# Performance work log

Hardware: AMD Instinct MI355X
Metric: run time of the kernel (lower is better)

The kernel has to match this reference:

```python
import jax, jax.numpy as jnp
import numpy as np

N_NODES = 100000
D_FEAT = 128            # per-embedding width; concat of 4 -> 512
INPUT_DIM = 4 * D_FEAT
HIDDEN_DIM = 64
N_SAMPLES = 250000


def _glorot(key, fan_in, fan_out):
    r = np.sqrt(6.0 / fan_in).astype(np.float32)
    return jax.random.uniform(key, (fan_in, fan_out), minval=-r, maxval=r, dtype=jnp.float32)


def setup_inputs() -> dict:
    key = jax.random.key(0)
    k1, k2, k3, k4, k5 = jax.random.split(key, 5)
    input1 = jax.random.normal(k1, (N_NODES, D_FEAT), dtype=jnp.float32)
    input2 = jax.random.normal(k2, (N_NODES, D_FEAT), dtype=jnp.float32)
    train_sample = jax.random.randint(k3, (N_SAMPLES, 2), 0, N_NODES, dtype=jnp.int64)
    w1 = _glorot(k4, INPUT_DIM, HIDDEN_DIM)
    b1 = jnp.zeros((HIDDEN_DIM,), dtype=jnp.float32)
    w2 = _glorot(k5, HIDDEN_DIM, 1)
    return {"input1": input1, "input2": input2, "train_sample": train_sample,
            "w1": w1, "b1": b1, "w2": w2}


def reference(input1, input2, train_sample, w1, b1, w2):
    src = train_sample[:, 0]
    dst = train_sample[:, 1]
    # four gathers + concat -> [E, 4*D_FEAT]
    h = jnp.concatenate([input1[src], input1[dst], input2[src], input2[dst]], axis=1)
    x = jax.nn.relu(h @ w1 + b1)          # [E, HIDDEN_DIM]
    return x @ w2                          # [E, 1]
```

## Files before the change

### kernel.cpp

```cpp
#include <hip/hip_runtime.h>
#include <hip/hip_bf16.h>

#define NN  100000
#define DF  128
#define HD  64
#define NS  250000


typedef __attribute__((ext_vector_type(8))) short bfrag;
typedef __attribute__((ext_vector_type(4))) float ffrag;

__device__ __forceinline__ unsigned short bf16bits(float f) {
    __hip_bfloat16 b = __float2bfloat16(f);
    return *(unsigned short*)&b;
}
__device__ __forceinline__ unsigned pack2(float a, float b) {
    return (unsigned)bf16bits(a) | ((unsigned)bf16bits(b) << 16);
}
__device__ __forceinline__ float bflo(unsigned u) {
    union { unsigned i; float f; } c; c.i = u << 16; return c.f;
}
__device__ __forceinline__ float bfhi(unsigned u) {
    union { unsigned i; float f; } c; c.i = u & 0xffff0000u; return c.f;
}

__global__ __launch_bounds__(256) void prep_w1_kernel(
    const float* __restrict__ w1, unsigned short* __restrict__ Bf)
{
    const int gid  = blockIdx.x * 256 + threadIdx.x;
    const int lane = gid & 63;
    const int ks   = (gid >> 6) & 7;
    const int tn   = gid >> 9;

    const int n     = tn * 16 + (lane & 15);
    const int kbase = ks * 32 + (lane >> 4) * 8;
    const int col   = n & 63;

    uint4 u;
    unsigned p[4];
    #pragma unroll
    for (int jp = 0; jp < 4; ++jp) {
        float v[2];
        #pragma unroll
        for (int h = 0; h < 2; ++h) {
            const int k = kbase + jp * 2 + h;
            const int row = ((k >= 128) ? 256 : 0) + ((n >= 64) ? 128 : 0) + (k & 127);
            v[h] = w1[(size_t)row * HD + col];
        }
        p[jp] = pack2(v[0], v[1]);
    }
    u.x = p[0]; u.y = p[1]; u.z = p[2]; u.w = p[3];
    *(uint4*)(Bf + (size_t)gid * 8) = u;
}

__global__ __launch_bounds__(256) void node_gemm_mfma(
    const float* __restrict__ in1,
    const float* __restrict__ in2,
    const unsigned short* __restrict__ Bf,
    unsigned short* __restrict__ Pn)
{
    __shared__ unsigned short smem[4096];

    const int t  = threadIdx.x;
    const int m0 = blockIdx.x * 16;

    {
        const int r  = t >> 4;
        const int qq = t & 15;
        const float* src = (qq < 8)
            ? in1 + (size_t)(m0 + r) * DF + qq * 16
            : in2 + (size_t)(m0 + r) * DF + (qq - 8) * 16;
        const float4 f0 = *(const float4*)(src);
        const float4 f1 = *(const float4*)(src + 4);
        const float4 f2 = *(const float4*)(src + 8);
        const float4 f3 = *(const float4*)(src + 12);
        uint4 u0, u1;
        u0.x = pack2(f0.x, f0.y); u0.y = pack2(f0.z, f0.w);
        u0.z = pack2(f1.x, f1.y); u0.w = pack2(f1.z, f1.w);
        u1.x = pack2(f2.x, f2.y); u1.y = pack2(f2.z, f2.w);
        u1.z = pack2(f3.x, f3.y); u1.w = pack2(f3.z, f3.w);
        const int g0 = qq * 2, g1 = qq * 2 + 1;
        *(uint4*)(&smem[(g0 >> 2) * 512 + ((g0 & 3) * 16 + r) * 8]) = u0;
        *(uint4*)(&smem[(g1 >> 2) * 512 + ((g1 & 3) * 16 + r) * 8]) = u1;
    }
    __syncthreads();

    const int lane = t & 63;
    const int w    = t >> 6;

    bfrag bf[2][8];
    #pragma unroll
    for (int ti = 0; ti < 2; ++ti) {
        const int tn = w * 2 + ti;
        #pragma unroll
        for (int ks = 0; ks < 8; ++ks)
            bf[ti][ks] = *(const bfrag*)(Bf + ((size_t)(tn * 8 + ks) * 64 + lane) * 8);
    }

    bfrag af[8];
    #pragma unroll
    for (int ks = 0; ks < 8; ++ks)
        af[ks] = *(const bfrag*)(&smem[ks * 512 + lane * 8]);

    ffrag acc[2] = {{0.f, 0.f, 0.f, 0.f}, {0.f, 0.f, 0.f, 0.f}};
    #pragma unroll
    for (int ks = 0; ks < 8; ++ks) {
        acc[0] = __builtin_amdgcn_mfma_f32_16x16x32_bf16(af[ks], bf[0][ks], acc[0], 0, 0, 0);
        acc[1] = __builtin_amdgcn_mfma_f32_16x16x32_bf16(af[ks], bf[1][ks], acc[1], 0, 0, 0);
    }

    __syncthreads();
    {
        const int col = lane & 15;
        const int rq  = lane >> 4;
        #pragma unroll
        for (int ti = 0; ti < 2; ++ti) {
            const int nc = (w * 2 + ti) * 16 + col;
            #pragma unroll
            for (int reg = 0; reg < 4; ++reg)
                smem[(rq * 4 + reg) * 128 + nc] = bf16bits(acc[ti][reg]);
        }
    }
    __syncthreads();
    {
        const int row = t >> 4;
        const int seg = t & 15;
        const uint4 u = *(const uint4*)(&smem[row * 128 + seg * 8]);
        *(uint4*)(Pn + (size_t)(m0 + row) * 128 + seg * 8) = u;
    }
}

__global__ __launch_bounds__(256) void edge_mlp_kernel(
    const unsigned short* __restrict__ Pn,
    const int*   __restrict__ ts,
    const float* __restrict__ b1,
    const float* __restrict__ w2,
    float* __restrict__ out)
{
    const int t = threadIdx.x;
    const int s = blockIdx.x * 16 + (t >> 4);
    const int l = t & 15;
    const int j = l * 4;

    const int2 e = ((const int2*)ts)[s];
    const uint2 uu = *(const uint2*)(Pn + (size_t)e.x * 128 + j);
    const uint2 vv = *(const uint2*)(Pn + (size_t)e.y * 128 + 64 + j);
    const float4 bb = *(const float4*)(b1 + j);
    const float4 ww = *(const float4*)(w2 + j);

    float p = 0.f, x;
    x = bflo(uu.x) + bflo(vv.x) + bb.x; x = x > 0.f ? x : 0.f; p += x * ww.x;
    x = bfhi(uu.x) + bfhi(vv.x) + bb.y; x = x > 0.f ? x : 0.f; p += x * ww.y;
    x = bflo(uu.y) + bflo(vv.y) + bb.z; x = x > 0.f ? x : 0.f; p += x * ww.z;
    x = bfhi(uu.y) + bfhi(vv.y) + bb.w; x = x > 0.f ? x : 0.f; p += x * ww.w;

    p += __shfl_xor(p, 1);
    p += __shfl_xor(p, 2);
    p += __shfl_xor(p, 4);
    p += __shfl_xor(p, 8);
    if (l == 0) out[s] = p;
}

extern "C" void kernel_launch(void* const* d_in, const int* in_sizes, int n_in,
                              void* d_out, int out_size, void* d_ws, size_t ws_size,
                              hipStream_t stream) {
    const float* in1 = (const float*)d_in[0];
    const float* in2 = (const float*)d_in[1];
    const int*   ts  = (const int*)  d_in[2];
    const float* w1  = (const float*)d_in[3];
    const float* b1  = (const float*)d_in[4];
    const float* w2  = (const float*)d_in[5];
    float* out = (float*)d_out;

    unsigned short* Pn = (unsigned short*)d_ws;
    const size_t Pbytes = (size_t)NN * 128 * sizeof(unsigned short);
    unsigned short* Bf;
    if (ws_size >= Pbytes + 65536)
        Bf = (unsigned short*)((char*)d_ws + Pbytes);
    else
        Bf = (unsigned short*)d_out;

    prep_w1_kernel<<<16, 256, 0, stream>>>(w1, Bf);
    node_gemm_mfma<<<NN / 16, 256, 0, stream>>>(in1, in2, Bf, Pn);
    edge_mlp_kernel<<<NS / 16, 256, 0, stream>>>(Pn, ts, b1, w2, out);
}
```

Before: 158.7 us.

## Process 80 nodes per block in node GEMM and widen edge loads

The node GEMM now handles five 16-row tiles per block. It loads the W1 fragments into registers once and reuses them across all five tiles, so the per-block weight reload cost is spread over more rows. The edge kernel now gives each sample 8 lanes with 16-byte loads instead of 16 lanes with 8-byte loads, which cuts shuffle steps and raises bytes per memory request. The trade-off is larger LDS use (40KB) and more registers per block, which may reduce occupancy, plus a bounds check for the edge tail.

```diff
diff --git a/kernel.cpp b/kernel.cpp
--- a/kernel.cpp
+++ b/kernel.cpp
@@ -59,54 +59,61 @@
     const unsigned short* __restrict__ Bf,
     unsigned short* __restrict__ Pn)
 {
-    __shared__ unsigned short smem[4096];
+    __shared__ unsigned short smem[20480];
 
     const int t  = threadIdx.x;
-    const int m0 = blockIdx.x * 16;
+    const int m0 = blockIdx.x * 80;
+
+    const int lane = t & 63;
+    const int w    = t >> 6;
+    bfrag bfr[2][8];
+    #pragma unroll
+    for (int ti = 0; ti < 2; ++ti) {
+        const int tn = w * 2 + ti;
+        #pragma unroll
+        for (int ks = 0; ks < 8; ++ks)
+            bfr[ti][ks] = *(const bfrag*)(Bf + ((size_t)(tn * 8 + ks) * 64 + lane) * 8);
+    }
 
     {
         const int r  = t >> 4;
         const int qq = t & 15;
-        const float* src = (qq < 8)
-            ? in1 + (size_t)(m0 + r) * DF + qq * 16
-            : in2 + (size_t)(m0 + r) * DF + (qq - 8) * 16;
-        const float4 f0 = *(const float4*)(src);
-        const float4 f1 = *(const float4*)(src + 4);
-        const float4 f2 = *(const float4*)(src + 8);
-        const float4 f3 = *(const float4*)(src + 12);
-        uint4 u0, u1;
-        u0.x = pack2(f0.x, f0.y); u0.y = pack2(f0.z, f0.w);
-        u0.z = pack2(f1.x, f1.y); u0.w = pack2(f1.z, f1.w);
-        u1.x = pack2(f2.x, f2.y); u1.y = pack2(f2.z, f2.w);
-        u1.z = pack2(f3.x, f3.y); u1.w = pack2(f3.z, f3.w);
-        const int g0 = qq * 2, g1 = qq * 2 + 1;
-        *(uint4*)(&smem[(g0 >> 2) * 512 + ((g0 & 3) * 16 + r) * 8]) = u0;
-        *(uint4*)(&smem[(g1 >> 2) * 512 + ((g1 & 3) * 16 + r) * 8]) = u1;
+        #pragma unroll
+        for (int st = 0; st < 5; ++st) {
+            const int row = m0 + st * 16 + r;
+            const float* src = (qq < 8)
+                ? in1 + (size_t)row * DF + qq * 16
+                : in2 + (size_t)row * DF + (qq - 8) * 16;
+            const float4 f0 = *(const float4*)(src);
+            const float4 f1 = *(const float4*)(src + 4);
+            const float4 f2 = *(const float4*)(src + 8);
+            const float4 f3 = *(const float4*)(src + 12);
+            uint4 u0, u1;
+            u0.x = pack2(f0.x, f0.y); u0.y = pack2(f0.z, f0.w);
+            u0.z = pack2(f1.x, f1.y); u0.w = pack2(f1.z, f1.w);
+            u1.x = pack2(f2.x, f2.y); u1.y = pack2(f2.z, f2.w);
+            u1.z = pack2(f3.x, f3.y); u1.w = pack2(f3.z, f3.w);
+            const int g0 = qq * 2, g1 = qq * 2 + 1;
+            *(uint4*)(&smem[st * 4096 + (g0 >> 2) * 512 + ((g0 & 3) * 16 + r) * 8]) = u0;
+            *(uint4*)(&smem[st * 4096 + (g1 >> 2) * 512 + ((g1 & 3) * 16 + r) * 8]) = u1;
+        }
     }
     __syncthreads();
 
-    const int lane = t & 63;
-    const int w    = t >> 6;
-
-    bfrag bf[2][8];
-    #pragma unroll
-    for (int ti = 0; ti < 2; ++ti) {
-        const int tn = w * 2 + ti;
-        #pragma unroll
-        for (int ks = 0; ks < 8; ++ks)
-            bf[ti][ks] = *(const bfrag*)(Bf + ((size_t)(tn * 8 + ks) * 64 + lane) * 8);
-    }
-
-    bfrag af[8];
-    #pragma unroll
-    for (int ks = 0; ks < 8; ++ks)
-        af[ks] = *(const bfrag*)(&smem[ks * 512 + lane * 8]);
-
-    ffrag acc[2] = {{0.f, 0.f, 0.f, 0.f}, {0.f, 0.f, 0.f, 0.f}};
+    ffrag acc[5][2];
+    #pragma unroll
+    for (int st = 0; st < 5; ++st) {
+        acc[st][0] = (ffrag){0.f, 0.f, 0.f, 0.f};
+        acc[st][1] = (ffrag){0.f, 0.f, 0.f, 0.f};
+    }
     #pragma unroll
     for (int ks = 0; ks < 8; ++ks) {
-        acc[0] = __builtin_amdgcn_mfma_f32_16x16x32_bf16(af[ks], bf[0][ks], acc[0], 0, 0, 0);
-        acc[1] = __builtin_amdgcn_mfma_f32_16x16x32_bf16(af[ks], bf[1][ks], acc[1], 0, 0, 0);
+        #pragma unroll
+        for (int st = 0; st < 5; ++st) {
+            const bfrag af = *(const bfrag*)(&smem[st * 4096 + ks * 512 + lane * 8]);
+            acc[st][0] = __builtin_amdgcn_mfma_f32_16x16x32_bf16(af, bfr[0][ks], acc[st][0], 0, 0, 0);
+            acc[st][1] = __builtin_amdgcn_mfma_f32_16x16x32_bf16(af, bfr[1][ks], acc[st][1], 0, 0, 0);
+        }
     }
 
     __syncthreads();
@@ -114,19 +121,26 @@
         const int col = lane & 15;
         const int rq  = lane >> 4;
         #pragma unroll
-        for (int ti = 0; ti < 2; ++ti) {
-            const int nc = (w * 2 + ti) * 16 + col;
+        for (int st = 0; st < 5; ++st) {
             #pragma unroll
-            for (int reg = 0; reg < 4; ++reg)
-                smem[(rq * 4 + reg) * 128 + nc] = bf16bits(acc[ti][reg]);
+            for (int ti = 0; ti < 2; ++ti) {
+                const int nc = (w * 2 + ti) * 16 + col;
+                #pragma unroll
+                for (int reg = 0; reg < 4; ++reg)
+                    smem[(st * 16 + rq * 4 + reg) * 128 + nc] = bf16bits(acc[st][ti][reg]);
+            }
         }
     }
     __syncthreads();
     {
-        const int row = t >> 4;
-        const int seg = t & 15;
-        const uint4 u = *(const uint4*)(&smem[row * 128 + seg * 8]);
-        *(uint4*)(Pn + (size_t)(m0 + row) * 128 + seg * 8) = u;
+        #pragma unroll
+        for (int i = 0; i < 5; ++i) {
+            const int idx = i * 256 + t;
+            const int row = idx >> 4;
+            const int seg = idx & 15;
+            const uint4 u = *(const uint4*)(&smem[row * 128 + seg * 8]);
+            *(uint4*)(Pn + (size_t)(m0 + row) * 128 + seg * 8) = u;
+        }
     }
 }
 
@@ -137,28 +151,34 @@
     const float* __restrict__ w2,
     float* __restrict__ out)
 {
-    const int t = threadIdx.x;
-    const int s = blockIdx.x * 16 + (t >> 4);
-    const int l = t & 15;
-    const int j = l * 4;
+    const int t  = threadIdx.x;
+    const int sr = blockIdx.x * 32 + (t >> 3);
+    const int s  = min(sr, NS - 1);
+    const int l  = t & 7;
+    const int j  = l * 8;
 
     const int2 e = ((const int2*)ts)[s];
-    const uint2 uu = *(const uint2*)(Pn + (size_t)e.x * 128 + j);
-    const uint2 vv = *(const uint2*)(Pn + (size_t)e.y * 128 + 64 + j);
-    const float4 bb = *(const float4*)(b1 + j);
-    const float4 ww = *(const float4*)(w2 + j);
+    const uint4 uu = *(const uint4*)(Pn + (size_t)e.x * 128 + j);
+    const uint4 vv = *(const uint4*)(Pn + (size_t)e.y * 128 + 64 + j);
+    const float4 b0 = *(const float4*)(b1 + j);
+    const float4 b4 = *(const float4*)(b1 + j + 4);
+    const float4 w0 = *(const float4*)(w2 + j);
+    const float4 w4 = *(const float4*)(w2 + j + 4);
 
     float p = 0.f, x;
-    x = bflo(uu.x) + bflo(vv.x) + bb.x; x = x > 0.f ? x : 0.f; p += x * ww.x;
-    x = bfhi(uu.x) + bfhi(vv.x) + bb.y; x = x > 0.f ? x : 0.f; p += x * ww.y;
-    x = bflo(uu.y) + bflo(vv.y) + bb.z; x = x > 0.f ? x : 0.f; p += x * ww.z;
-    x = bfhi(uu.y) + bfhi(vv.y) + bb.w; x = x > 0.f ? x : 0.f; p += x * ww.w;
+    x = bflo(uu.x) + bflo(vv.x) + b0.x; x = x > 0.f ? x : 0.f; p += x * w0.x;
+    x = bfhi(uu.x) + bfhi(vv.x) + b0.y; x = x > 0.f ? x : 0.f; p += x * w0.y;
+    x = bflo(uu.y) + bflo(vv.y) + b0.z; x = x > 0.f ? x : 0.f; p += x * w0.z;
+    x = bfhi(uu.y) + bfhi(vv.y) + b0.w; x = x > 0.f ? x : 0.f; p += x * w0.w;
+    x = bflo(uu.z) + bflo(vv.z) + b4.x; x = x > 0.f ? x : 0.f; p += x * w4.x;
+    x = bfhi(uu.z) + bfhi(vv.z) + b4.y; x = x > 0.f ? x : 0.f; p += x * w4.y;
+    x = bflo(uu.w) + bflo(vv.w) + b4.z; x = x > 0.f ? x : 0.f; p += x * w4.z;
+    x = bfhi(uu.w) + bfhi(vv.w) + b4.w; x = x > 0.f ? x : 0.f; p += x * w4.w;
 
     p += __shfl_xor(p, 1);
     p += __shfl_xor(p, 2);
     p += __shfl_xor(p, 4);
-    p += __shfl_xor(p, 8);
-    if (l == 0) out[s] = p;
+    if (l == 0 && sr < NS) out[sr] = p;
 }
 
 extern "C" void kernel_launch(void* const* d_in, const int* in_sizes, int n_in,
@@ -181,6 +201,6 @@
         Bf = (unsigned short*)d_out;
 
     prep_w1_kernel<<<16, 256, 0, stream>>>(w1, Bf);
-    node_gemm_mfma<<<NN / 16, 256, 0, stream>>>(in1, in2, Bf, Pn);
-    edge_mlp_kernel<<<NS / 16, 256, 0, stream>>>(Pn, ts, b1, w2, out);
-}
+    node_gemm_mfma<<<NN / 80, 256, 0, stream>>>(in1, in2, Bf, Pn);
+    edge_mlp_kernel<<<(NS + 31) / 32, 256, 0, stream>>>(Pn, ts, b1, w2, out);
+}
```

New measurement: 147.7 us. 1.07x faster.
